# Performance work log

Measured on AMD Instinct MI355X. Metric: run time of the kernel, lower is better.

The kernel has to match this reference:

```python
import jax, jax.numpy as jnp
import numpy as np

LN_EPS = 1e-5


def setup_inputs() -> dict:
    key = jax.random.key(0)
    ks = jax.random.split(key, 7)
    B, L, D, H = 1, 4096, 512, 8  # batch must be 1; d_k=d_v=d_model (see source's double-bmm)
    q = jax.random.normal(ks[0], (B, L, D), jnp.float32)
    k = jax.random.normal(ks[1], (B, L, D), jnp.float32)
    v = jax.random.normal(ks[2], (B, L, D), jnp.float32)
    # causal mask: True = masked (filled with -inf), guarantees no fully-masked row
    attn_mask = jnp.triu(jnp.ones((L, L), dtype=bool), k=1)[None]  # (1, L, L)
    # xavier-normal-ish init for per-head projections (H, d_model, d_k)
    wscale = np.float32(np.sqrt(2.0 / (D + D)))
    w_qs = jax.random.normal(ks[3], (H, D, D), jnp.float32) * wscale
    w_ks = jax.random.normal(ks[4], (H, D, D), jnp.float32) * wscale
    w_vs = jax.random.normal(ks[5], (H, D, D), jnp.float32) * wscale
    pscale = np.float32(np.sqrt(2.0 / (H * D + D)))
    proj_w = jax.random.normal(ks[6], (D, H * D), jnp.float32) * pscale  # Linear(H*d_v, d_model)
    proj_b = jnp.zeros((D,), jnp.float32)
    ln_gamma = jnp.ones((D,), jnp.float32)
    ln_beta = jnp.zeros((D,), jnp.float32)
    return dict(q=q, k=k, v=v, attn_mask=attn_mask, w_qs=w_qs, w_ks=w_ks, w_vs=w_vs,
                proj_w=proj_w, proj_b=proj_b, ln_gamma=ln_gamma, ln_beta=ln_beta)


def reference(q, k, v, attn_mask, w_qs, w_ks, w_vs, proj_w, proj_b, ln_gamma, ln_beta):
    H, D, Dk = w_qs.shape          # d_k == d_model (required by source's duplicated bmm)
    B, Lq, _ = q.shape             # B == 1 (required by source's duplicated bmm)
    temper = jnp.sqrt(jnp.asarray(D, q.dtype))

    def proj_twice(x, w):
        # first projection: repeat over heads then bmm -> (H, B*L, Dk) -> view (H*B, L, Dk)
        xs = jnp.einsum('bld,hdk->hblk', x, w).reshape(H * B, -1, Dk)
        # duplicated second projection (faithful to the source code)
        return jnp.einsum('hlm,hmk->hlk', xs, w)  # (H, L, Dk)

    q_s = proj_twice(q, w_qs)
    k_s = proj_twice(k, w_ks)
    v_s = proj_twice(v, w_vs)

    # naive attention: full (H, Lq, Lk) score matrix materialized
    scores = jnp.einsum('hqd,hkd->hqk', q_s, k_s) / temper
    mask = jnp.broadcast_to(attn_mask, scores.shape)  # mask.repeat(n_head,1,1) with B=1
    scores = jnp.where(mask, -jnp.inf, scores)
    attn = jax.nn.softmax(scores, axis=-1)            # dropout = identity (eval mode)
    heads = jnp.einsum('hqk,hkd->hqd', attn, v_s)     # (H, Lq, Dv)

    # split along batch dim then cat along feature dim == (B, Lq, H*Dv)
    out = heads.transpose(1, 0, 2).reshape(B, Lq, H * Dk)
    out = out @ proj_w.T + proj_b                     # final Linear; dropout = identity

    x = out + q                                       # residual
    mu = jnp.mean(x, axis=-1, keepdims=True)
    var = jnp.var(x, axis=-1, keepdims=True)
    out = (x - mu) / jnp.sqrt(var + LN_EPS) * ln_gamma + ln_beta
    return out, attn
```

## Files before the change

kernel.cpp:

```cpp
#include <hip/hip_runtime.h>


typedef _Float16 f16;
typedef __attribute__((ext_vector_type(8))) _Float16 half8;
typedef __attribute__((ext_vector_type(4))) float float4v;

#define LSEQ 4096
#define DMODEL 512
#define NHEAD 8
#define BKK 64
#define LDSK (BKK + 8)

__device__ __forceinline__ half8 load8h(const f16* p) { return *(const half8*)p; }
__device__ __forceinline__ half8 load8h(const float* p) {
    float4 a = *(const float4*)p;
    float4 b = *(const float4*)(p + 4);
    half8 r;
    r[0] = (f16)a.x; r[1] = (f16)a.y; r[2] = (f16)a.z; r[3] = (f16)a.w;
    r[4] = (f16)b.x; r[5] = (f16)b.y; r[6] = (f16)b.z; r[7] = (f16)b.w;
    return r;
}

template<typename TA, typename TB, int BLAYOUT, int OUTMODE, bool KLIMIT>
__launch_bounds__(256)
__global__ void gemm64_kernel(const TA* __restrict__ A,
                              const TB* __restrict__ B,
                              void* __restrict__ Cv,
                              int M, int N, int K,
                              int ldA, int ldB, int ldC,
                              long sA, long sB, long sC,
                              float scale)
{
    const int bz = blockIdx.z;
    const int n0 = blockIdx.x * 64;
    const int m0 = blockIdx.y * 64;
    const int tid  = threadIdx.x;
    const int lane = tid & 63;
    const int wave = tid >> 6;
    const int wr = wave >> 1, wc = wave & 1;
    const int quad = lane >> 4, lr = lane & 15;

    if (OUTMODE == 2) {
        if (n0 >= m0 + 64) {
            float* Cb = (float*)Cv + (long)bz * sC;
            const float ninf = -__builtin_inff();
            float4 vv = make_float4(ninf, ninf, ninf, ninf);
            int r = tid >> 2, c = (tid & 3) * 16;
            #pragma unroll
            for (int j = 0; j < 4; j++)
                *(float4*)&Cb[(long)(m0 + r) * ldC + n0 + c + j * 4] = vv;
            return;
        }
    }

    __shared__ __align__(16) f16 Asm[64 * LDSK];
    __shared__ __align__(16) f16 Bsm[64 * LDSK];

    A += (long)bz * sA;
    B += (long)bz * sB;

    float4v acc[2][2];
    #pragma unroll
    for (int i = 0; i < 2; i++)
        #pragma unroll
        for (int j = 0; j < 2; j++) acc[i][j] = (float4v)0.0f;

    int kend = K;
    if (KLIMIT) kend = min(K, m0 + 64);

    const int rA = tid >> 3;
    const int cA = (tid & 7) * 8;

    for (int k0 = 0; k0 < kend; k0 += BKK) {
        {
            half8 v0 = load8h(&A[(long)(m0 + rA)      * ldA + k0 + cA]);
            half8 v1 = load8h(&A[(long)(m0 + rA + 32) * ldA + k0 + cA]);
            *(half8*)&Asm[ rA       * LDSK + cA] = v0;
            *(half8*)&Asm[(rA + 32) * LDSK + cA] = v1;
        }
        if (BLAYOUT == 0) {
            half8 v0 = load8h(&B[(long)(n0 + rA)      * ldB + k0 + cA]);
            half8 v1 = load8h(&B[(long)(n0 + rA + 32) * ldB + k0 + cA]);
            *(half8*)&Bsm[ rA       * LDSK + cA] = v0;
            *(half8*)&Bsm[(rA + 32) * LDSK + cA] = v1;
        } else {
            half8 v0 = load8h(&B[(long)(k0 + rA)      * ldB + n0 + cA]);
            half8 v1 = load8h(&B[(long)(k0 + rA + 32) * ldB + n0 + cA]);
            #pragma unroll
            for (int j = 0; j < 8; j++) {
                Bsm[(cA + j) * LDSK + rA     ] = v0[j];
                Bsm[(cA + j) * LDSK + rA + 32] = v1[j];
            }
        }
        __syncthreads();

        #pragma unroll
        for (int ks = 0; ks < 2; ks++) {
            half8 af[2], bfv[2];
            #pragma unroll
            for (int mt = 0; mt < 2; mt++)
                af[mt] = *(const half8*)&Asm[(wr * 32 + mt * 16 + lr) * LDSK + ks * 32 + quad * 8];
            #pragma unroll
            for (int nt = 0; nt < 2; nt++)
                bfv[nt] = *(const half8*)&Bsm[(wc * 32 + nt * 16 + lr) * LDSK + ks * 32 + quad * 8];
            #pragma unroll
            for (int mt = 0; mt < 2; mt++)
                #pragma unroll
                for (int nt = 0; nt < 2; nt++)
                    acc[mt][nt] = __builtin_amdgcn_mfma_f32_16x16x32_f16(
                        af[mt], bfv[nt], acc[mt][nt], 0, 0, 0);
        }
        __syncthreads();
    }

    #pragma unroll
    for (int mt = 0; mt < 2; mt++) {
        #pragma unroll
        for (int nt = 0; nt < 2; nt++) {
            #pragma unroll
            for (int r = 0; r < 4; r++) {
                int row = m0 + wr * 32 + mt * 16 + quad * 4 + r;
                int col = n0 + wc * 32 + nt * 16 + lr;
                float val = acc[mt][nt][r] * scale;
                if (OUTMODE == 0) {
                    f16* Cb = (f16*)Cv + (long)bz * sC;
                    Cb[(long)row * ldC + col] = (f16)val;
                } else if (OUTMODE == 1) {
                    float* Cb = (float*)Cv + (long)bz * sC;
                    Cb[(long)row * ldC + col] = val;
                } else {
                    float* Cb = (float*)Cv + (long)bz * sC;
                    if (col > row) val = -__builtin_inff();
                    Cb[(long)row * ldC + col] = val;
                }
            }
        }
    }
}

__launch_bounds__(256)
__global__ void softmax_kernel(float* __restrict__ attn)
{
    __shared__ float s[LSEQ];
    __shared__ float red[8];
    const long row = blockIdx.x;
    float* p = attn + row * (long)LSEQ;
    const int tid = threadIdx.x;

    float lmax = -__builtin_inff();
    #pragma unroll
    for (int i = 0; i < 4; i++) {
        float4 v = *(const float4*)&p[tid * 16 + i * 4];
        s[tid * 16 + i * 4 + 0] = v.x;
        s[tid * 16 + i * 4 + 1] = v.y;
        s[tid * 16 + i * 4 + 2] = v.z;
        s[tid * 16 + i * 4 + 3] = v.w;
        lmax = fmaxf(lmax, fmaxf(fmaxf(v.x, v.y), fmaxf(v.z, v.w)));
    }
    #pragma unroll
    for (int off = 32; off > 0; off >>= 1) lmax = fmaxf(lmax, __shfl_down(lmax, off));
    if ((tid & 63) == 0) red[tid >> 6] = lmax;
    __syncthreads();
    const float m = fmaxf(fmaxf(red[0], red[1]), fmaxf(red[2], red[3]));
    __syncthreads();

    float lsum = 0.0f;
    #pragma unroll
    for (int j = 0; j < 16; j++) {
        float e = __expf(s[tid * 16 + j] - m);
        s[tid * 16 + j] = e;
        lsum += e;
    }
    #pragma unroll
    for (int off = 32; off > 0; off >>= 1) lsum += __shfl_down(lsum, off);
    if ((tid & 63) == 0) red[tid >> 6] = lsum;
    __syncthreads();
    const float inv = 1.0f / (red[0] + red[1] + red[2] + red[3]);

    #pragma unroll
    for (int i = 0; i < 4; i++) {
        float4 o;
        o.x = s[tid * 16 + i * 4 + 0] * inv;
        o.y = s[tid * 16 + i * 4 + 1] * inv;
        o.z = s[tid * 16 + i * 4 + 2] * inv;
        o.w = s[tid * 16 + i * 4 + 3] * inv;
        *(float4*)&p[tid * 16 + i * 4] = o;
    }
}

__launch_bounds__(256)
__global__ void ln_kernel(float* lin_out,
                          const float* __restrict__ qin,
                          const float* __restrict__ bias,
                          const float* __restrict__ gamma,
                          const float* __restrict__ beta)
{
    __shared__ float red[8];
    const int l = blockIdx.x;
    const int tid = threadIdx.x;
    float* pl = lin_out + (long)l * DMODEL;
    const float* pq = qin + (long)l * DMODEL;

    float x0 = pl[tid]       + pq[tid]       + bias[tid];
    float x1 = pl[tid + 256] + pq[tid + 256] + bias[tid + 256];
    float sum = x0 + x1, sq = x0 * x0 + x1 * x1;
    #pragma unroll
    for (int off = 32; off > 0; off >>= 1) {
        sum += __shfl_down(sum, off);
        sq  += __shfl_down(sq,  off);
    }
    if ((tid & 63) == 0) { red[tid >> 6] = sum; red[4 + (tid >> 6)] = sq; }
    __syncthreads();
    const float S  = red[0] + red[1] + red[2] + red[3];
    const float Q2 = red[4] + red[5] + red[6] + red[7];
    const float mu = S * (1.0f / DMODEL);
    const float var = Q2 * (1.0f / DMODEL) - mu * mu;
    const float rstd = rsqrtf(var + 1e-5f);

    pl[tid]       = (x0 - mu) * rstd * gamma[tid]       + beta[tid];
    pl[tid + 256] = (x1 - mu) * rstd * gamma[tid + 256] + beta[tid + 256];
}

extern "C" void kernel_launch(void* const* d_in, const int* in_sizes, int n_in,
                              void* d_out, int out_size, void* d_ws, size_t ws_size,
                              hipStream_t stream)
{
    const float* q      = (const float*)d_in[0];
    const float* k      = (const float*)d_in[1];
    const float* v      = (const float*)d_in[2];
    const float* w_qs   = (const float*)d_in[4];
    const float* w_ks   = (const float*)d_in[5];
    const float* w_vs   = (const float*)d_in[6];
    const float* proj_w = (const float*)d_in[7];
    const float* proj_b = (const float*)d_in[8];
    const float* gamma  = (const float*)d_in[9];
    const float* beta   = (const float*)d_in[10];

    float* out  = (float*)d_out;
    float* attn = (float*)d_out + (long)LSEQ * DMODEL;

    const long PROJ = (long)NHEAD * LSEQ * DMODEL;
    char* ws = (char*)d_ws;
    f16* q_s   = (f16*)ws;  ws += PROJ * 2;
    f16* k_s   = (f16*)ws;  ws += PROJ * 2;
    f16* v_s   = (f16*)ws;  ws += PROJ * 2;
    f16* heads = (f16*)ws;

    f16* w2 = (f16*)d_out;

    const dim3 blk(256);
    const float inv_temper = 0.044194173824159216f;
    const long sW  = (long)DMODEL * DMODEL;
    const long sT  = (long)LSEQ * DMODEL;

    const dim3 gW(DMODEL / 64, DMODEL / 64, NHEAD);
    const dim3 gP(DMODEL / 64, LSEQ / 64, NHEAD);
    gemm64_kernel<float, float, 1, 0, false><<<gW, blk, 0, stream>>>(w_qs, w_qs, w2,  DMODEL, DMODEL, DMODEL, DMODEL, DMODEL, DMODEL, sW, sW, sW, 1.0f);
    gemm64_kernel<float, f16,   1, 0, false><<<gP, blk, 0, stream>>>(q,    w2,   q_s, LSEQ,   DMODEL, DMODEL, DMODEL, DMODEL, DMODEL, 0,  sW, sT, 1.0f);
    gemm64_kernel<float, float, 1, 0, false><<<gW, blk, 0, stream>>>(w_ks, w_ks, w2,  DMODEL, DMODEL, DMODEL, DMODEL, DMODEL, DMODEL, sW, sW, sW, 1.0f);
    gemm64_kernel<float, f16,   1, 0, false><<<gP, blk, 0, stream>>>(k,    w2,   k_s, LSEQ,   DMODEL, DMODEL, DMODEL, DMODEL, DMODEL, 0,  sW, sT, 1.0f);
    gemm64_kernel<float, float, 1, 0, false><<<gW, blk, 0, stream>>>(w_vs, w_vs, w2,  DMODEL, DMODEL, DMODEL, DMODEL, DMODEL, DMODEL, sW, sW, sW, 1.0f);
    gemm64_kernel<float, f16,   1, 0, false><<<gP, blk, 0, stream>>>(v,    w2,   v_s, LSEQ,   DMODEL, DMODEL, DMODEL, DMODEL, DMODEL, 0,  sW, sT, 1.0f);

    const dim3 gS(LSEQ / 64, LSEQ / 64, NHEAD);
    gemm64_kernel<f16, f16, 0, 2, false><<<gS, blk, 0, stream>>>(
        q_s, k_s, attn, LSEQ, LSEQ, DMODEL,
        DMODEL, DMODEL, LSEQ,
        sT, sT, (long)LSEQ * LSEQ, inv_temper);

    softmax_kernel<<<dim3(NHEAD * LSEQ), blk, 0, stream>>>(attn);

    gemm64_kernel<float, f16, 1, 0, true><<<dim3(DMODEL / 64, LSEQ / 64, NHEAD), blk, 0, stream>>>(
        attn, v_s, heads, LSEQ, DMODEL, LSEQ,
        LSEQ, DMODEL, NHEAD * DMODEL,
        (long)LSEQ * LSEQ, sT, (long)DMODEL, 1.0f);

    gemm64_kernel<f16, float, 0, 1, false><<<dim3(DMODEL / 64, LSEQ / 64, 1), blk, 0, stream>>>(
        heads, proj_w, out, LSEQ, DMODEL, NHEAD * DMODEL,
        NHEAD * DMODEL, NHEAD * DMODEL, DMODEL,
        0, 0, 0, 1.0f);

    ln_kernel<<<dim3(LSEQ), blk, 0, stream>>>(out, q, proj_b, gamma, beta);
}
```

Baseline: 1.775 ms.

## Fuse softmax with P·V product and store V projection transposed

Replaces the separate softmax and attn·V GEMM kernels with one kernel. Each block takes 32 query rows of one head, computes the row max and sum online over the causal range only, then writes normalized probabilities back and feeds them as fp16 through LDS into MFMA against a transposed V. The V projection now writes its output transposed so the fused kernel can read contiguous key-dimension slices. Fully masked score tiles are now written as zeros rather than -inf, which matches the final softmax output. The aim is to cut the repeated reads and writes of the 512MB score matrix and skip the masked upper triangle. The cost is that each block computes a full 512-wide output per row tile, and the transposed scattered fp16 stores in the V projection are uncoalesced.

```diff
diff --git a/kernel.cpp b/kernel.cpp
--- a/kernel.cpp
+++ b/kernel.cpp
@@ -43,8 +43,7 @@
     if (OUTMODE == 2) {
         if (n0 >= m0 + 64) {
             float* Cb = (float*)Cv + (long)bz * sC;
-            const float ninf = -__builtin_inff();
-            float4 vv = make_float4(ninf, ninf, ninf, ninf);
+            float4 vv = make_float4(0.0f, 0.0f, 0.0f, 0.0f);
             int r = tid >> 2, c = (tid & 3) * 16;
             #pragma unroll
             for (int j = 0; j < 4; j++)
@@ -128,6 +127,9 @@
                 } else if (OUTMODE == 1) {
                     float* Cb = (float*)Cv + (long)bz * sC;
                     Cb[(long)row * ldC + col] = val;
+                } else if (OUTMODE == 3) {
+                    f16* Cb = (f16*)Cv + (long)bz * sC;
+                    Cb[(long)col * ldC + row] = (f16)val;
                 } else {
                     float* Cb = (float*)Cv + (long)bz * sC;
                     if (col > row) val = -__builtin_inff();
@@ -139,53 +141,105 @@
 }
 
 __launch_bounds__(256)
-__global__ void softmax_kernel(float* __restrict__ attn)
+__global__ void softmax_pv_kernel(float* __restrict__ attn,
+                                  const f16* __restrict__ vT,
+                                  f16* __restrict__ heads)
 {
-    __shared__ float s[LSEQ];
-    __shared__ float red[8];
-    const long row = blockIdx.x;
-    float* p = attn + row * (long)LSEQ;
-    const int tid = threadIdx.x;
-
-    float lmax = -__builtin_inff();
-    #pragma unroll
-    for (int i = 0; i < 4; i++) {
-        float4 v = *(const float4*)&p[tid * 16 + i * 4];
-        s[tid * 16 + i * 4 + 0] = v.x;
-        s[tid * 16 + i * 4 + 1] = v.y;
-        s[tid * 16 + i * 4 + 2] = v.z;
-        s[tid * 16 + i * 4 + 3] = v.w;
-        lmax = fmaxf(lmax, fmaxf(fmaxf(v.x, v.y), fmaxf(v.z, v.w)));
-    }
-    #pragma unroll
-    for (int off = 32; off > 0; off >>= 1) lmax = fmaxf(lmax, __shfl_down(lmax, off));
-    if ((tid & 63) == 0) red[tid >> 6] = lmax;
+    int g = blockIdx.x;
+    int mb, h;
+    if (g < 512) { mb = g >> 2;                 h = g & 3; }
+    else         { g -= 512; mb = 127 - (g >> 2); h = 4 + (g & 3); }
+    const int m0 = mb * 32;
+    const int KE = (m0 & ~63) + 64;
+
+    const int tid  = threadIdx.x;
+    const int lane = tid & 63;
+    const int wc   = tid >> 6;
+    const int quad = lane >> 4, lr = lane & 15;
+
+    __shared__ __align__(16) f16 Psm[32 * LDSK];
+    __shared__ float mrow[32], isrow[32];
+
+    float* S = attn + (long)h * LSEQ * LSEQ;
+    const int r   = tid >> 3;
+    const int sub = tid & 7;
+    float* prow = S + (long)(m0 + r) * LSEQ;
+
+    float mt = -1e30f, st = 0.0f;
+    for (int k = sub * 8; k < KE; k += 64) {
+        float4 a = *(const float4*)&prow[k];
+        float4 b = *(const float4*)&prow[k + 4];
+        float mx = fmaxf(fmaxf(fmaxf(a.x, a.y), fmaxf(a.z, a.w)),
+                         fmaxf(fmaxf(b.x, b.y), fmaxf(b.z, b.w)));
+        if (mx > mt) { st *= __expf(mt - mx); mt = mx; }
+        st += __expf(a.x - mt) + __expf(a.y - mt) + __expf(a.z - mt) + __expf(a.w - mt)
+            + __expf(b.x - mt) + __expf(b.y - mt) + __expf(b.z - mt) + __expf(b.w - mt);
+    }
+    #pragma unroll
+    for (int off = 1; off < 8; off <<= 1) {
+        float mo = __shfl_xor(mt, off);
+        float so = __shfl_xor(st, off);
+        float mn = fmaxf(mt, mo);
+        st = st * __expf(mt - mn) + so * __expf(mo - mn);
+        mt = mn;
+    }
+    if (sub == 0) { mrow[r] = mt; isrow[r] = 1.0f / st; }
     __syncthreads();
-    const float m = fmaxf(fmaxf(red[0], red[1]), fmaxf(red[2], red[3]));
-    __syncthreads();
-
-    float lsum = 0.0f;
-    #pragma unroll
-    for (int j = 0; j < 16; j++) {
-        float e = __expf(s[tid * 16 + j] - m);
-        s[tid * 16 + j] = e;
-        lsum += e;
-    }
-    #pragma unroll
-    for (int off = 32; off > 0; off >>= 1) lsum += __shfl_down(lsum, off);
-    if ((tid & 63) == 0) red[tid >> 6] = lsum;
-    __syncthreads();
-    const float inv = 1.0f / (red[0] + red[1] + red[2] + red[3]);
-
-    #pragma unroll
-    for (int i = 0; i < 4; i++) {
-        float4 o;
-        o.x = s[tid * 16 + i * 4 + 0] * inv;
-        o.y = s[tid * 16 + i * 4 + 1] * inv;
-        o.z = s[tid * 16 + i * 4 + 2] * inv;
-        o.w = s[tid * 16 + i * 4 + 3] * inv;
-        *(float4*)&p[tid * 16 + i * 4] = o;
-    }
+    const float m_r = mrow[r], is_r = isrow[r];
+
+    float4v acc[2][8];
+    #pragma unroll
+    for (int i = 0; i < 2; i++)
+        #pragma unroll
+        for (int j = 0; j < 8; j++) acc[i][j] = (float4v)0.0f;
+
+    for (int kt = 0; kt < KE; kt += 64) {
+        float* pk = prow + kt + sub * 8;
+        float4 a = *(const float4*)pk;
+        float4 b = *(const float4*)(pk + 4);
+        a.x = __expf(a.x - m_r) * is_r;  a.y = __expf(a.y - m_r) * is_r;
+        a.z = __expf(a.z - m_r) * is_r;  a.w = __expf(a.w - m_r) * is_r;
+        b.x = __expf(b.x - m_r) * is_r;  b.y = __expf(b.y - m_r) * is_r;
+        b.z = __expf(b.z - m_r) * is_r;  b.w = __expf(b.w - m_r) * is_r;
+        *(float4*)pk = a;
+        *(float4*)(pk + 4) = b;
+        half8 hp;
+        hp[0] = (f16)a.x; hp[1] = (f16)a.y; hp[2] = (f16)a.z; hp[3] = (f16)a.w;
+        hp[4] = (f16)b.x; hp[5] = (f16)b.y; hp[6] = (f16)b.z; hp[7] = (f16)b.w;
+        *(half8*)&Psm[r * LDSK + sub * 8] = hp;
+        __syncthreads();
+
+        half8 af[2][2];
+        #pragma unroll
+        for (int m2 = 0; m2 < 2; m2++)
+            #pragma unroll
+            for (int ks = 0; ks < 2; ks++)
+                af[m2][ks] = *(const half8*)&Psm[(m2 * 16 + lr) * LDSK + ks * 32 + quad * 8];
+
+        const f16* vb = vT + ((long)h * DMODEL + wc * 128) * LSEQ + kt + quad * 8;
+        #pragma unroll
+        for (int nt = 0; nt < 8; nt++) {
+            const f16* vp = vb + (long)(nt * 16 + lr) * LSEQ;
+            half8 b0 = *(const half8*)vp;
+            half8 b1 = *(const half8*)(vp + 32);
+            acc[0][nt] = __builtin_amdgcn_mfma_f32_16x16x32_f16(af[0][0], b0, acc[0][nt], 0, 0, 0);
+            acc[0][nt] = __builtin_amdgcn_mfma_f32_16x16x32_f16(af[0][1], b1, acc[0][nt], 0, 0, 0);
+            acc[1][nt] = __builtin_amdgcn_mfma_f32_16x16x32_f16(af[1][0], b0, acc[1][nt], 0, 0, 0);
+            acc[1][nt] = __builtin_amdgcn_mfma_f32_16x16x32_f16(af[1][1], b1, acc[1][nt], 0, 0, 0);
+        }
+        __syncthreads();
+    }
+
+    #pragma unroll
+    for (int m2 = 0; m2 < 2; m2++)
+        #pragma unroll
+        for (int nt = 0; nt < 8; nt++)
+            #pragma unroll
+            for (int rr = 0; rr < 4; rr++) {
+                int row = m0 + m2 * 16 + quad * 4 + rr;
+                int col = wc * 128 + nt * 16 + lr;
+                heads[(long)row * (NHEAD * DMODEL) + h * DMODEL + col] = (f16)acc[m2][nt][rr];
+            }
 }
 
 __launch_bounds__(256)
@@ -243,7 +297,7 @@
     char* ws = (char*)d_ws;
     f16* q_s   = (f16*)ws;  ws += PROJ * 2;
     f16* k_s   = (f16*)ws;  ws += PROJ * 2;
-    f16* v_s   = (f16*)ws;  ws += PROJ * 2;
+    f16* v_sT  = (f16*)ws;  ws += PROJ * 2;
     f16* heads = (f16*)ws;
 
     f16* w2 = (f16*)d_out;
@@ -260,7 +314,7 @@
     gemm64_kernel<float, float, 1, 0, false><<<gW, blk, 0, stream>>>(w_ks, w_ks, w2,  DMODEL, DMODEL, DMODEL, DMODEL, DMODEL, DMODEL, sW, sW, sW, 1.0f);
     gemm64_kernel<float, f16,   1, 0, false><<<gP, blk, 0, stream>>>(k,    w2,   k_s, LSEQ,   DMODEL, DMODEL, DMODEL, DMODEL, DMODEL, 0,  sW, sT, 1.0f);
     gemm64_kernel<float, float, 1, 0, false><<<gW, blk, 0, stream>>>(w_vs, w_vs, w2,  DMODEL, DMODEL, DMODEL, DMODEL, DMODEL, DMODEL, sW, sW, sW, 1.0f);
-    gemm64_kernel<float, f16,   1, 0, false><<<gP, blk, 0, stream>>>(v,    w2,   v_s, LSEQ,   DMODEL, DMODEL, DMODEL, DMODEL, DMODEL, 0,  sW, sT, 1.0f);
+    gemm64_kernel<float, f16,   1, 3, false><<<gP, blk, 0, stream>>>(v,    w2,   v_sT, LSEQ,  DMODEL, DMODEL, DMODEL, DMODEL, LSEQ,   0,  sW, sT, 1.0f);
 
     const dim3 gS(LSEQ / 64, LSEQ / 64, NHEAD);
     gemm64_kernel<f16, f16, 0, 2, false><<<gS, blk, 0, stream>>>(
@@ -268,12 +322,7 @@
         DMODEL, DMODEL, LSEQ,
         sT, sT, (long)LSEQ * LSEQ, inv_temper);
 
-    softmax_kernel<<<dim3(NHEAD * LSEQ), blk, 0, stream>>>(attn);
-
-    gemm64_kernel<float, f16, 1, 0, true><<<dim3(DMODEL / 64, LSEQ / 64, NHEAD), blk, 0, stream>>>(
-        attn, v_s, heads, LSEQ, DMODEL, LSEQ,
-        LSEQ, DMODEL, NHEAD * DMODEL,
-        (long)LSEQ * LSEQ, sT, (long)DMODEL, 1.0f);
+    softmax_pv_kernel<<<dim3(128 * NHEAD), blk, 0, stream>>>(attn, v_sT, heads);
 
     gemm64_kernel<f16, float, 0, 1, false><<<dim3(DMODEL / 64, LSEQ / 64, 1), blk, 0, stream>>>(
         heads, proj_w, out, LSEQ, DMODEL, NHEAD * DMODEL,
```

Measured after the change: 1.552 ms. 12.6% less time.

## Fuse QK^T, softmax and PV into a two-pass flash-style attention kernel

Applied to the files above, without the earlier changes.

Replaces the separate score GEMM, row softmax kernel and attn×V GEMM with a single kernel per 32-row query block and head. The kernel computes the row max and sum in a first pass over causal key tiles, then recomputes scores, writes the normalized attention probabilities and accumulates P·V with MFMA in a second pass. The V projection now writes a transposed V, and the temperature scale is folded into the Q projection. The aim is to avoid reading back the full fp32 score matrix for softmax and again for PV, and to skip masked tiles beyond the diagonal except for zero-filling them. In exchange, QK^T is computed twice, and K and V are loaded directly from global memory without shared-memory staging.

```diff
diff --git a/kernel.cpp b/kernel.cpp
--- a/kernel.cpp
+++ b/kernel.cpp
@@ -10,6 +10,10 @@
 #define NHEAD 8
 #define BKK 64
 #define LDSK (BKK + 8)
+#define QLD (DMODEL + 8)
+#define PLD (128 + 8)
+#define MASKV -3.0e38f
+#define MINIT -1.0e30f
 
 __device__ __forceinline__ half8 load8h(const f16* p) { return *(const half8*)p; }
 __device__ __forceinline__ half8 load8h(const float* p) {
@@ -21,7 +25,7 @@
     return r;
 }
 
-template<typename TA, typename TB, int BLAYOUT, int OUTMODE, bool KLIMIT>
+template<typename TA, typename TB, int BLAYOUT, int OUTMODE>
 __launch_bounds__(256)
 __global__ void gemm64_kernel(const TA* __restrict__ A,
                               const TB* __restrict__ B,
@@ -40,19 +44,6 @@
     const int wr = wave >> 1, wc = wave & 1;
     const int quad = lane >> 4, lr = lane & 15;
 
-    if (OUTMODE == 2) {
-        if (n0 >= m0 + 64) {
-            float* Cb = (float*)Cv + (long)bz * sC;
-            const float ninf = -__builtin_inff();
-            float4 vv = make_float4(ninf, ninf, ninf, ninf);
-            int r = tid >> 2, c = (tid & 3) * 16;
-            #pragma unroll
-            for (int j = 0; j < 4; j++)
-                *(float4*)&Cb[(long)(m0 + r) * ldC + n0 + c + j * 4] = vv;
-            return;
-        }
-    }
-
     __shared__ __align__(16) f16 Asm[64 * LDSK];
     __shared__ __align__(16) f16 Bsm[64 * LDSK];
 
@@ -65,13 +56,10 @@
         #pragma unroll
         for (int j = 0; j < 2; j++) acc[i][j] = (float4v)0.0f;
 
-    int kend = K;
-    if (KLIMIT) kend = min(K, m0 + 64);
-
     const int rA = tid >> 3;
     const int cA = (tid & 7) * 8;
 
-    for (int k0 = 0; k0 < kend; k0 += BKK) {
+    for (int k0 = 0; k0 < K; k0 += BKK) {
         {
             half8 v0 = load8h(&A[(long)(m0 + rA)      * ldA + k0 + cA]);
             half8 v1 = load8h(&A[(long)(m0 + rA + 32) * ldA + k0 + cA]);
@@ -113,6 +101,25 @@
         __syncthreads();
     }
 
+    if (OUTMODE == 3) {
+        #pragma unroll
+        for (int mt = 0; mt < 2; mt++)
+            #pragma unroll
+            for (int nt = 0; nt < 2; nt++)
+                #pragma unroll
+                for (int r = 0; r < 4; r++) {
+                    int rl = wr * 32 + mt * 16 + quad * 4 + r;
+                    int cl = wc * 32 + nt * 16 + lr;
+                    Asm[cl * LDSK + rl] = (f16)(acc[mt][nt][r] * scale);
+                }
+        __syncthreads();
+        f16* Cb = (f16*)Cv + (long)bz * sC;
+        int cl = tid >> 2, rch = (tid & 3) * 16;
+        *(half8*)&Cb[(long)(n0 + cl) * ldC + m0 + rch]     = *(const half8*)&Asm[cl * LDSK + rch];
+        *(half8*)&Cb[(long)(n0 + cl) * ldC + m0 + rch + 8] = *(const half8*)&Asm[cl * LDSK + rch + 8];
+        return;
+    }
+
     #pragma unroll
     for (int mt = 0; mt < 2; mt++) {
         #pragma unroll
@@ -125,12 +132,8 @@
                 if (OUTMODE == 0) {
                     f16* Cb = (f16*)Cv + (long)bz * sC;
                     Cb[(long)row * ldC + col] = (f16)val;
-                } else if (OUTMODE == 1) {
-                    float* Cb = (float*)Cv + (long)bz * sC;
-                    Cb[(long)row * ldC + col] = val;
                 } else {
                     float* Cb = (float*)Cv + (long)bz * sC;
-                    if (col > row) val = -__builtin_inff();
                     Cb[(long)row * ldC + col] = val;
                 }
             }
@@ -139,53 +142,215 @@
 }
 
 __launch_bounds__(256)
-__global__ void softmax_kernel(float* __restrict__ attn)
+__global__ void flash_kernel(const f16* __restrict__ q_s,
+                             const f16* __restrict__ k_s,
+                             const f16* __restrict__ vT,
+                             float* __restrict__ attn,
+                             f16* __restrict__ heads)
 {
-    __shared__ float s[LSEQ];
-    __shared__ float red[8];
-    const long row = blockIdx.x;
-    float* p = attn + row * (long)LSEQ;
-    const int tid = threadIdx.x;
-
-    float lmax = -__builtin_inff();
-    #pragma unroll
-    for (int i = 0; i < 4; i++) {
-        float4 v = *(const float4*)&p[tid * 16 + i * 4];
-        s[tid * 16 + i * 4 + 0] = v.x;
-        s[tid * 16 + i * 4 + 1] = v.y;
-        s[tid * 16 + i * 4 + 2] = v.z;
-        s[tid * 16 + i * 4 + 3] = v.w;
-        lmax = fmaxf(lmax, fmaxf(fmaxf(v.x, v.y), fmaxf(v.z, v.w)));
-    }
-    #pragma unroll
-    for (int off = 32; off > 0; off >>= 1) lmax = fmaxf(lmax, __shfl_down(lmax, off));
-    if ((tid & 63) == 0) red[tid >> 6] = lmax;
+    const int g = blockIdx.x;
+    const int h = g & 7;
+    const int j = g >> 3;
+    const int mb = (j & 1) ? (127 - (j >> 1)) : (j >> 1);
+    const int m0 = mb * 32;
+    const int KE2 = (m0 & ~127) + 128;
+
+    const int tid  = threadIdx.x;
+    const int w    = tid >> 6;
+    const int lane = tid & 63;
+    const int quad = lane >> 4, lr = lane & 15;
+
+    __shared__ __align__(16) f16 Qsm[32 * QLD];
+    __shared__ __align__(16) f16 Psm[2][32 * PLD];
+    __shared__ float warrM[4][32], warrL[4][32];
+    __shared__ float mrow[32], isrow[32];
+
+    const long sT  = (long)LSEQ * DMODEL;
+    float* A = attn + (long)h * LSEQ * LSEQ;
+
+    {
+        const int zr = tid >> 3, zc = (tid & 7) * 16;
+        const float4 z = make_float4(0.0f, 0.0f, 0.0f, 0.0f);
+        for (int kt = KE2; kt < LSEQ; kt += 128) {
+            float* p = A + (long)(m0 + zr) * LSEQ + kt + zc;
+            *(float4*)p = z; *(float4*)(p + 4) = z;
+            *(float4*)(p + 8) = z; *(float4*)(p + 12) = z;
+        }
+    }
+
+    {
+        const f16* qp = q_s + (long)h * sT + (long)m0 * DMODEL;
+        const int rq = tid >> 3, cq = (tid & 7) * 8;
+        #pragma unroll
+        for (int jj = 0; jj < 8; jj++)
+            *(half8*)&Qsm[rq * QLD + cq + jj * 64] =
+                *(const half8*)&qp[(long)rq * DMODEL + cq + jj * 64];
+    }
     __syncthreads();
-    const float m = fmaxf(fmaxf(red[0], red[1]), fmaxf(red[2], red[3]));
+
+    const f16* kbase = k_s + (long)h * sT + (long)(32 * w + lr) * DMODEL;
+
+    float m8[8], l8[8];
+    #pragma unroll
+    for (int i = 0; i < 8; i++) { m8[i] = MINIT; l8[i] = 0.0f; }
+
+    for (int kt = 0; kt < KE2; kt += 128) {
+        float4v s[2][2];
+        #pragma unroll
+        for (int mf = 0; mf < 2; mf++)
+            #pragma unroll
+            for (int nf = 0; nf < 2; nf++) s[mf][nf] = (float4v)0.0f;
+
+        const f16* kp0 = kbase + (long)kt * DMODEL;
+        const f16* kp1 = kp0 + 16 * DMODEL;
+        #pragma unroll
+        for (int ks = 0; ks < 16; ks++) {
+            half8 a0 = *(const half8*)&Qsm[lr        * QLD + ks * 32 + quad * 8];
+            half8 a1 = *(const half8*)&Qsm[(lr + 16) * QLD + ks * 32 + quad * 8];
+            half8 b0 = *(const half8*)&kp0[ks * 32 + quad * 8];
+            half8 b1 = *(const half8*)&kp1[ks * 32 + quad * 8];
+            s[0][0] = __builtin_amdgcn_mfma_f32_16x16x32_f16(a0, b0, s[0][0], 0, 0, 0);
+            s[0][1] = __builtin_amdgcn_mfma_f32_16x16x32_f16(a0, b1, s[0][1], 0, 0, 0);
+            s[1][0] = __builtin_amdgcn_mfma_f32_16x16x32_f16(a1, b0, s[1][0], 0, 0, 0);
+            s[1][1] = __builtin_amdgcn_mfma_f32_16x16x32_f16(a1, b1, s[1][1], 0, 0, 0);
+        }
+        const bool domask = (kt + 128 == KE2);
+        #pragma unroll
+        for (int mf = 0; mf < 2; mf++)
+            #pragma unroll
+            for (int nf = 0; nf < 2; nf++)
+                #pragma unroll
+                for (int rr = 0; rr < 4; rr++) {
+                    float v = s[mf][nf][rr];
+                    if (domask &&
+                        (kt + 32 * w + 16 * nf + lr > m0 + 16 * mf + quad * 4 + rr))
+                        v = MASKV;
+                    const int i = mf * 4 + rr;
+                    if (v <= m8[i]) {
+                        l8[i] += __expf(v - m8[i]);
+                    } else {
+                        l8[i] = l8[i] * __expf(m8[i] - v) + 1.0f;
+                        m8[i] = v;
+                    }
+                }
+    }
+
+    #pragma unroll
+    for (int off = 1; off < 16; off <<= 1) {
+        #pragma unroll
+        for (int i = 0; i < 8; i++) {
+            float mo = __shfl_xor(m8[i], off);
+            float lo = __shfl_xor(l8[i], off);
+            float nm = fmaxf(m8[i], mo);
+            l8[i] = l8[i] * __expf(m8[i] - nm) + lo * __expf(mo - nm);
+            m8[i] = nm;
+        }
+    }
+    if (lr == 0) {
+        #pragma unroll
+        for (int i = 0; i < 8; i++) {
+            const int rl = 16 * (i >> 2) + quad * 4 + (i & 3);
+            warrM[w][rl] = m8[i]; warrL[w][rl] = l8[i];
+        }
+    }
     __syncthreads();
-
-    float lsum = 0.0f;
-    #pragma unroll
-    for (int j = 0; j < 16; j++) {
-        float e = __expf(s[tid * 16 + j] - m);
-        s[tid * 16 + j] = e;
-        lsum += e;
-    }
-    #pragma unroll
-    for (int off = 32; off > 0; off >>= 1) lsum += __shfl_down(lsum, off);
-    if ((tid & 63) == 0) red[tid >> 6] = lsum;
+    if (tid < 32) {
+        float m = MINIT, l = 0.0f;
+        #pragma unroll
+        for (int ww = 0; ww < 4; ww++) {
+            float mo = warrM[ww][tid], lo = warrL[ww][tid];
+            float nm = fmaxf(m, mo);
+            l = l * __expf(m - nm) + lo * __expf(mo - nm);
+            m = nm;
+        }
+        mrow[tid] = m; isrow[tid] = 1.0f / l;
+    }
     __syncthreads();
-    const float inv = 1.0f / (red[0] + red[1] + red[2] + red[3]);
-
-    #pragma unroll
-    for (int i = 0; i < 4; i++) {
-        float4 o;
-        o.x = s[tid * 16 + i * 4 + 0] * inv;
-        o.y = s[tid * 16 + i * 4 + 1] * inv;
-        o.z = s[tid * 16 + i * 4 + 2] * inv;
-        o.w = s[tid * 16 + i * 4 + 3] * inv;
-        *(float4*)&p[tid * 16 + i * 4] = o;
-    }
+
+    float mf8[8], if8[8];
+    #pragma unroll
+    for (int i = 0; i < 8; i++) {
+        const int rl = 16 * (i >> 2) + quad * 4 + (i & 3);
+        mf8[i] = mrow[rl]; if8[i] = isrow[rl];
+    }
+
+    float4v acc[2][8];
+    #pragma unroll
+    for (int mf = 0; mf < 2; mf++)
+        #pragma unroll
+        for (int nt = 0; nt < 8; nt++) acc[mf][nt] = (float4v)0.0f;
+
+    int buf = 0;
+    for (int kt = 0; kt < KE2; kt += 128) {
+        float4v s[2][2];
+        #pragma unroll
+        for (int mf = 0; mf < 2; mf++)
+            #pragma unroll
+            for (int nf = 0; nf < 2; nf++) s[mf][nf] = (float4v)0.0f;
+
+        const f16* kp0 = kbase + (long)kt * DMODEL;
+        const f16* kp1 = kp0 + 16 * DMODEL;
+        #pragma unroll
+        for (int ks = 0; ks < 16; ks++) {
+            half8 a0 = *(const half8*)&Qsm[lr        * QLD + ks * 32 + quad * 8];
+            half8 a1 = *(const half8*)&Qsm[(lr + 16) * QLD + ks * 32 + quad * 8];
+            half8 b0 = *(const half8*)&kp0[ks * 32 + quad * 8];
+            half8 b1 = *(const half8*)&kp1[ks * 32 + quad * 8];
+            s[0][0] = __builtin_amdgcn_mfma_f32_16x16x32_f16(a0, b0, s[0][0], 0, 0, 0);
+            s[0][1] = __builtin_amdgcn_mfma_f32_16x16x32_f16(a0, b1, s[0][1], 0, 0, 0);
+            s[1][0] = __builtin_amdgcn_mfma_f32_16x16x32_f16(a1, b0, s[1][0], 0, 0, 0);
+            s[1][1] = __builtin_amdgcn_mfma_f32_16x16x32_f16(a1, b1, s[1][1], 0, 0, 0);
+        }
+        const bool domask = (kt + 128 == KE2);
+        #pragma unroll
+        for (int mf = 0; mf < 2; mf++)
+            #pragma unroll
+            for (int nf = 0; nf < 2; nf++)
+                #pragma unroll
+                for (int rr = 0; rr < 4; rr++) {
+                    float v = s[mf][nf][rr];
+                    if (domask &&
+                        (kt + 32 * w + 16 * nf + lr > m0 + 16 * mf + quad * 4 + rr))
+                        v = MASKV;
+                    const int i = mf * 4 + rr;
+                    const float p = __expf(v - mf8[i]) * if8[i];
+                    const int rl = 16 * mf + quad * 4 + rr;
+                    A[(long)(m0 + rl) * LSEQ + kt + 32 * w + 16 * nf + lr] = p;
+                    Psm[buf][rl * PLD + 32 * w + 16 * nf + lr] = (f16)p;
+                }
+        __syncthreads();
+
+        half8 af[2][4];
+        #pragma unroll
+        for (int mf = 0; mf < 2; mf++)
+            #pragma unroll
+            for (int ksv = 0; ksv < 4; ksv++)
+                af[mf][ksv] = *(const half8*)&Psm[buf][(16 * mf + lr) * PLD + ksv * 32 + quad * 8];
+
+        const f16* vbase = vT + ((long)h * DMODEL + 128 * w) * LSEQ + kt;
+        #pragma unroll
+        for (int nt = 0; nt < 8; nt++) {
+            const f16* vp = vbase + (long)(nt * 16 + lr) * LSEQ;
+            #pragma unroll
+            for (int ksv = 0; ksv < 4; ksv++) {
+                half8 bv = *(const half8*)&vp[ksv * 32 + quad * 8];
+                acc[0][nt] = __builtin_amdgcn_mfma_f32_16x16x32_f16(af[0][ksv], bv, acc[0][nt], 0, 0, 0);
+                acc[1][nt] = __builtin_amdgcn_mfma_f32_16x16x32_f16(af[1][ksv], bv, acc[1][nt], 0, 0, 0);
+            }
+        }
+        buf ^= 1;
+    }
+
+    #pragma unroll
+    for (int mf = 0; mf < 2; mf++)
+        #pragma unroll
+        for (int nt = 0; nt < 8; nt++)
+            #pragma unroll
+            for (int rr = 0; rr < 4; rr++) {
+                const int row = m0 + 16 * mf + quad * 4 + rr;
+                const int col = 128 * w + nt * 16 + lr;
+                heads[(long)row * (NHEAD * DMODEL) + h * DMODEL + col] = (f16)acc[mf][nt][rr];
+            }
 }
 
 __launch_bounds__(256)
@@ -243,7 +408,7 @@
     char* ws = (char*)d_ws;
     f16* q_s   = (f16*)ws;  ws += PROJ * 2;
     f16* k_s   = (f16*)ws;  ws += PROJ * 2;
-    f16* v_s   = (f16*)ws;  ws += PROJ * 2;
+    f16* v_sT  = (f16*)ws;  ws += PROJ * 2;
     f16* heads = (f16*)ws;
 
     f16* w2 = (f16*)d_out;
@@ -255,27 +420,16 @@
 
     const dim3 gW(DMODEL / 64, DMODEL / 64, NHEAD);
     const dim3 gP(DMODEL / 64, LSEQ / 64, NHEAD);
-    gemm64_kernel<float, float, 1, 0, false><<<gW, blk, 0, stream>>>(w_qs, w_qs, w2,  DMODEL, DMODEL, DMODEL, DMODEL, DMODEL, DMODEL, sW, sW, sW, 1.0f);
-    gemm64_kernel<float, f16,   1, 0, false><<<gP, blk, 0, stream>>>(q,    w2,   q_s, LSEQ,   DMODEL, DMODEL, DMODEL, DMODEL, DMODEL, 0,  sW, sT, 1.0f);
-    gemm64_kernel<float, float, 1, 0, false><<<gW, blk, 0, stream>>>(w_ks, w_ks, w2,  DMODEL, DMODEL, DMODEL, DMODEL, DMODEL, DMODEL, sW, sW, sW, 1.0f);
-    gemm64_kernel<float, f16,   1, 0, false><<<gP, blk, 0, stream>>>(k,    w2,   k_s, LSEQ,   DMODEL, DMODEL, DMODEL, DMODEL, DMODEL, 0,  sW, sT, 1.0f);
-    gemm64_kernel<float, float, 1, 0, false><<<gW, blk, 0, stream>>>(w_vs, w_vs, w2,  DMODEL, DMODEL, DMODEL, DMODEL, DMODEL, DMODEL, sW, sW, sW, 1.0f);
-    gemm64_kernel<float, f16,   1, 0, false><<<gP, blk, 0, stream>>>(v,    w2,   v_s, LSEQ,   DMODEL, DMODEL, DMODEL, DMODEL, DMODEL, 0,  sW, sT, 1.0f);
-
-    const dim3 gS(LSEQ / 64, LSEQ / 64, NHEAD);
-    gemm64_kernel<f16, f16, 0, 2, false><<<gS, blk, 0, stream>>>(
-        q_s, k_s, attn, LSEQ, LSEQ, DMODEL,
-        DMODEL, DMODEL, LSEQ,
-        sT, sT, (long)LSEQ * LSEQ, inv_temper);
-
-    softmax_kernel<<<dim3(NHEAD * LSEQ), blk, 0, stream>>>(attn);
-
-    gemm64_kernel<float, f16, 1, 0, true><<<dim3(DMODEL / 64, LSEQ / 64, NHEAD), blk, 0, stream>>>(
-        attn, v_s, heads, LSEQ, DMODEL, LSEQ,
-        LSEQ, DMODEL, NHEAD * DMODEL,
-        (long)LSEQ * LSEQ, sT, (long)DMODEL, 1.0f);
-
-    gemm64_kernel<f16, float, 0, 1, false><<<dim3(DMODEL / 64, LSEQ / 64, 1), blk, 0, stream>>>(
+    gemm64_kernel<float, float, 1, 0><<<gW, blk, 0, stream>>>(w_qs, w_qs, w2,  DMODEL, DMODEL, DMODEL, DMODEL, DMODEL, DMODEL, sW, sW, sW, 1.0f);
+    gemm64_kernel<float, f16,   1, 0><<<gP, blk, 0, stream>>>(q,    w2,   q_s, LSEQ,   DMODEL, DMODEL, DMODEL, DMODEL, DMODEL, 0,  sW, sT, inv_temper);
+    gemm64_kernel<float, float, 1, 0><<<gW, blk, 0, stream>>>(w_ks, w_ks, w2,  DMODEL, DMODEL, DMODEL, DMODEL, DMODEL, DMODEL, sW, sW, sW, 1.0f);
+    gemm64_kernel<float, f16,   1, 0><<<gP, blk, 0, stream>>>(k,    w2,   k_s, LSEQ,   DMODEL, DMODEL, DMODEL, DMODEL, DMODEL, 0,  sW, sT, 1.0f);
+    gemm64_kernel<float, float, 1, 0><<<gW, blk, 0, stream>>>(w_vs, w_vs, w2,  DMODEL, DMODEL, DMODEL, DMODEL, DMODEL, DMODEL, sW, sW, sW, 1.0f);
+    gemm64_kernel<float, f16,   1, 3><<<gP, blk, 0, stream>>>(v,    w2,   v_sT, LSEQ,  DMODEL, DMODEL, DMODEL, DMODEL, LSEQ,   0,  sW, sT, 1.0f);
+
+    flash_kernel<<<dim3(128 * NHEAD), blk, 0, stream>>>(q_s, k_s, v_sT, attn, heads);
+
+    gemm64_kernel<f16, float, 0, 1><<<dim3(DMODEL / 64, LSEQ / 64, 1), blk, 0, stream>>>(
         heads, proj_w, out, LSEQ, DMODEL, NHEAD * DMODEL,
         NHEAD * DMODEL, NHEAD * DMODEL, DMODEL,
         0, 0, 0, 1.0f);
```

After: 2.685 ms. 51.2% more time.

## Fuse softmax normalization into PV kernel with per-row stats pass

Applied to the files above, without the earlier changes.

Replaces the full-row softmax kernel with a stats kernel that computes online max and inverse-sum only over the causal prefix, followed by a fused PV kernel. The PV kernel normalizes scores, writes the attention probabilities back in place and feeds them to MFMA against a transposed V. It also folds the temperature scale into the Q projection and writes zeros directly for masked tiles. This removes the separate read/write pass over the upper-triangular half of the 512MB attention matrix, at the cost of reading V from global memory without LDS reuse and a new transposed-output epilogue.

```diff
diff --git a/kernel.cpp b/kernel.cpp
--- a/kernel.cpp
+++ b/kernel.cpp
@@ -3,6 +3,7 @@
 
 typedef _Float16 f16;
 typedef __attribute__((ext_vector_type(8))) _Float16 half8;
+typedef __attribute__((ext_vector_type(4))) _Float16 half4;
 typedef __attribute__((ext_vector_type(4))) float float4v;
 
 #define LSEQ 4096
@@ -10,6 +11,8 @@
 #define NHEAD 8
 #define BKK 64
 #define LDSK (BKK + 8)
+#define PLD 80
+#define MINIT -1.0e30f
 
 __device__ __forceinline__ half8 load8h(const f16* p) { return *(const half8*)p; }
 __device__ __forceinline__ half8 load8h(const float* p) {
@@ -21,7 +24,7 @@
     return r;
 }
 
-template<typename TA, typename TB, int BLAYOUT, int OUTMODE, bool KLIMIT>
+template<typename TA, typename TB, int BLAYOUT, int OUTMODE>
 __launch_bounds__(256)
 __global__ void gemm64_kernel(const TA* __restrict__ A,
                               const TB* __restrict__ B,
@@ -43,8 +46,7 @@
     if (OUTMODE == 2) {
         if (n0 >= m0 + 64) {
             float* Cb = (float*)Cv + (long)bz * sC;
-            const float ninf = -__builtin_inff();
-            float4 vv = make_float4(ninf, ninf, ninf, ninf);
+            float4 vv = make_float4(0.0f, 0.0f, 0.0f, 0.0f);
             int r = tid >> 2, c = (tid & 3) * 16;
             #pragma unroll
             for (int j = 0; j < 4; j++)
@@ -65,13 +67,10 @@
         #pragma unroll
         for (int j = 0; j < 2; j++) acc[i][j] = (float4v)0.0f;
 
-    int kend = K;
-    if (KLIMIT) kend = min(K, m0 + 64);
-
     const int rA = tid >> 3;
     const int cA = (tid & 7) * 8;
 
-    for (int k0 = 0; k0 < kend; k0 += BKK) {
+    for (int k0 = 0; k0 < K; k0 += BKK) {
         {
             half8 v0 = load8h(&A[(long)(m0 + rA)      * ldA + k0 + cA]);
             half8 v1 = load8h(&A[(long)(m0 + rA + 32) * ldA + k0 + cA]);
@@ -113,6 +112,25 @@
         __syncthreads();
     }
 
+    if (OUTMODE == 3) {
+        #pragma unroll
+        for (int mt = 0; mt < 2; mt++)
+            #pragma unroll
+            for (int nt = 0; nt < 2; nt++)
+                #pragma unroll
+                for (int r = 0; r < 4; r++) {
+                    int rl = wr * 32 + mt * 16 + quad * 4 + r;
+                    int cl = wc * 32 + nt * 16 + lr;
+                    Asm[cl * LDSK + rl] = (f16)(acc[mt][nt][r] * scale);
+                }
+        __syncthreads();
+        f16* Cb = (f16*)Cv + (long)bz * sC;
+        int cl = tid >> 2, rch = (tid & 3) * 16;
+        *(half8*)&Cb[(long)(n0 + cl) * ldC + m0 + rch]     = *(const half8*)&Asm[cl * LDSK + rch];
+        *(half8*)&Cb[(long)(n0 + cl) * ldC + m0 + rch + 8] = *(const half8*)&Asm[cl * LDSK + rch + 8];
+        return;
+    }
+
     #pragma unroll
     for (int mt = 0; mt < 2; mt++) {
         #pragma unroll
@@ -125,12 +143,12 @@
                 if (OUTMODE == 0) {
                     f16* Cb = (f16*)Cv + (long)bz * sC;
                     Cb[(long)row * ldC + col] = (f16)val;
-                } else if (OUTMODE == 1) {
+                } else if (OUTMODE == 2) {
                     float* Cb = (float*)Cv + (long)bz * sC;
+                    if (col > row) val = -__builtin_inff();
                     Cb[(long)row * ldC + col] = val;
                 } else {
                     float* Cb = (float*)Cv + (long)bz * sC;
-                    if (col > row) val = -__builtin_inff();
                     Cb[(long)row * ldC + col] = val;
                 }
             }
@@ -139,53 +157,110 @@
 }
 
 __launch_bounds__(256)
-__global__ void softmax_kernel(float* __restrict__ attn)
-{
-    __shared__ float s[LSEQ];
-    __shared__ float red[8];
-    const long row = blockIdx.x;
-    float* p = attn + row * (long)LSEQ;
-    const int tid = threadIdx.x;
-
-    float lmax = -__builtin_inff();
-    #pragma unroll
-    for (int i = 0; i < 4; i++) {
-        float4 v = *(const float4*)&p[tid * 16 + i * 4];
-        s[tid * 16 + i * 4 + 0] = v.x;
-        s[tid * 16 + i * 4 + 1] = v.y;
-        s[tid * 16 + i * 4 + 2] = v.z;
-        s[tid * 16 + i * 4 + 3] = v.w;
-        lmax = fmaxf(lmax, fmaxf(fmaxf(v.x, v.y), fmaxf(v.z, v.w)));
-    }
-    #pragma unroll
-    for (int off = 32; off > 0; off >>= 1) lmax = fmaxf(lmax, __shfl_down(lmax, off));
-    if ((tid & 63) == 0) red[tid >> 6] = lmax;
+__global__ void stats_kernel(const float* __restrict__ attn,
+                             float2* __restrict__ ml)
+{
+    const int rl   = (blockIdx.x << 2) + (threadIdx.x >> 6);
+    const int lane = threadIdx.x & 63;
+    const int h = rl >> 12;
+    const int r = rl & (LSEQ - 1);
+    const float* p = attn + (long)h * LSEQ * LSEQ + (long)r * LSEQ;
+    const int KE = (r & ~63) + 64;
+
+    float m = MINIT, l = 0.0f;
+    for (int k = lane * 8; k < KE; k += 512) {
+        float4 a = *(const float4*)&p[k];
+        float4 b = *(const float4*)&p[k + 4];
+        float mx = fmaxf(fmaxf(fmaxf(a.x, a.y), fmaxf(a.z, a.w)),
+                         fmaxf(fmaxf(b.x, b.y), fmaxf(b.z, b.w)));
+        if (mx > m) { l *= __expf(m - mx); m = mx; }
+        l += __expf(a.x - m) + __expf(a.y - m) + __expf(a.z - m) + __expf(a.w - m)
+           + __expf(b.x - m) + __expf(b.y - m) + __expf(b.z - m) + __expf(b.w - m);
+    }
+    #pragma unroll
+    for (int off = 1; off < 64; off <<= 1) {
+        float mo = __shfl_xor(m, off);
+        float lo = __shfl_xor(l, off);
+        float nm = fmaxf(m, mo);
+        l = l * __expf(m - nm) + lo * __expf(mo - nm);
+        m = nm;
+    }
+    if (lane == 0) ml[rl] = make_float2(m, 1.0f / l);
+}
+
+__launch_bounds__(256)
+__global__ void pv_kernel(float* __restrict__ attn,
+                          const f16* __restrict__ vT,
+                          const float2* __restrict__ ml,
+                          f16* __restrict__ heads)
+{
+    const int x = blockIdx.x;
+    const int h = blockIdx.y;
+    const int mb = (x & 1) ? (255 - (x >> 1)) : (x >> 1);
+    const int m0 = mb * 16;
+    const int KE = (m0 & ~63) + 64;
+
+    const int tid  = threadIdx.x;
+    const int w    = tid >> 6;
+    const int lane = tid & 63;
+    const int quad = lane >> 4, lr = lane & 15;
+
+    __shared__ __align__(16) f16 Psm[2][16 * PLD];
+    __shared__ float mrow[16], irow[16];
+
+    if (tid < 16) {
+        float2 s = ml[h * LSEQ + m0 + tid];
+        mrow[tid] = s.x; irow[tid] = s.y;
+    }
     __syncthreads();
-    const float m = fmaxf(fmaxf(red[0], red[1]), fmaxf(red[2], red[3]));
-    __syncthreads();
-
-    float lsum = 0.0f;
-    #pragma unroll
-    for (int j = 0; j < 16; j++) {
-        float e = __expf(s[tid * 16 + j] - m);
-        s[tid * 16 + j] = e;
-        lsum += e;
-    }
-    #pragma unroll
-    for (int off = 32; off > 0; off >>= 1) lsum += __shfl_down(lsum, off);
-    if ((tid & 63) == 0) red[tid >> 6] = lsum;
-    __syncthreads();
-    const float inv = 1.0f / (red[0] + red[1] + red[2] + red[3]);
-
-    #pragma unroll
-    for (int i = 0; i < 4; i++) {
-        float4 o;
-        o.x = s[tid * 16 + i * 4 + 0] * inv;
-        o.y = s[tid * 16 + i * 4 + 1] * inv;
-        o.z = s[tid * 16 + i * 4 + 2] * inv;
-        o.w = s[tid * 16 + i * 4 + 3] * inv;
-        *(float4*)&p[tid * 16 + i * 4] = o;
-    }
+
+    float* A = attn + (long)h * LSEQ * LSEQ;
+    const int pr = tid >> 4;
+    const int pc = (tid & 15) * 4;
+    const float m_r = mrow[pr], i_r = irow[pr];
+
+    float4v acc[8];
+    #pragma unroll
+    for (int i = 0; i < 8; i++) acc[i] = (float4v)0.0f;
+
+    const f16* vbase = vT + ((long)h * DMODEL + 128 * w) * LSEQ;
+
+    int buf = 0;
+    for (int kt = 0; kt < KE; kt += 64) {
+        float* pp = A + (long)(m0 + pr) * LSEQ + kt + pc;
+        float4 a = *(const float4*)pp;
+        a.x = __expf(a.x - m_r) * i_r;
+        a.y = __expf(a.y - m_r) * i_r;
+        a.z = __expf(a.z - m_r) * i_r;
+        a.w = __expf(a.w - m_r) * i_r;
+        *(float4*)pp = a;
+        half4 hp;
+        hp[0] = (f16)a.x; hp[1] = (f16)a.y; hp[2] = (f16)a.z; hp[3] = (f16)a.w;
+        *(half4*)&Psm[buf][pr * PLD + pc] = hp;
+        __syncthreads();
+
+        half8 af0 = *(const half8*)&Psm[buf][lr * PLD + quad * 8];
+        half8 af1 = *(const half8*)&Psm[buf][lr * PLD + 32 + quad * 8];
+        const f16* vp = vbase + kt + quad * 8;
+        #pragma unroll
+        for (int nt = 0; nt < 8; nt++) {
+            const f16* vrow = vp + (long)(nt * 16 + lr) * LSEQ;
+            half8 b0 = *(const half8*)vrow;
+            half8 b1 = *(const half8*)(vrow + 32);
+            acc[nt] = __builtin_amdgcn_mfma_f32_16x16x32_f16(af0, b0, acc[nt], 0, 0, 0);
+            acc[nt] = __builtin_amdgcn_mfma_f32_16x16x32_f16(af1, b1, acc[nt], 0, 0, 0);
+        }
+        buf ^= 1;
+    }
+
+    #pragma unroll
+    for (int nt = 0; nt < 8; nt++)
+        #pragma unroll
+        for (int rr = 0; rr < 4; rr++) {
+            const int row = m0 + quad * 4 + rr;
+            const int col = 128 * w + nt * 16 + lr;
+            heads[(long)row * (NHEAD * DMODEL) + h * DMODEL + col] = (f16)acc[nt][rr];
+        }
 }
 
 __launch_bounds__(256)
@@ -243,10 +318,11 @@
     char* ws = (char*)d_ws;
     f16* q_s   = (f16*)ws;  ws += PROJ * 2;
     f16* k_s   = (f16*)ws;  ws += PROJ * 2;
-    f16* v_s   = (f16*)ws;  ws += PROJ * 2;
+    f16* v_sT  = (f16*)ws;  ws += PROJ * 2;
     f16* heads = (f16*)ws;
 
-    f16* w2 = (f16*)d_out;
+    f16* w2    = (f16*)d_out;
+    float2* ml = (float2*)((char*)d_out + (4 << 20));
 
     const dim3 blk(256);
     const float inv_temper = 0.044194173824159216f;
@@ -255,27 +331,24 @@
 
     const dim3 gW(DMODEL / 64, DMODEL / 64, NHEAD);
     const dim3 gP(DMODEL / 64, LSEQ / 64, NHEAD);
-    gemm64_kernel<float, float, 1, 0, false><<<gW, blk, 0, stream>>>(w_qs, w_qs, w2,  DMODEL, DMODEL, DMODEL, DMODEL, DMODEL, DMODEL, sW, sW, sW, 1.0f);
-    gemm64_kernel<float, f16,   1, 0, false><<<gP, blk, 0, stream>>>(q,    w2,   q_s, LSEQ,   DMODEL, DMODEL, DMODEL, DMODEL, DMODEL, 0,  sW, sT, 1.0f);
-    gemm64_kernel<float, float, 1, 0, false><<<gW, blk, 0, stream>>>(w_ks, w_ks, w2,  DMODEL, DMODEL, DMODEL, DMODEL, DMODEL, DMODEL, sW, sW, sW, 1.0f);
-    gemm64_kernel<float, f16,   1, 0, false><<<gP, blk, 0, stream>>>(k,    w2,   k_s, LSEQ,   DMODEL, DMODEL, DMODEL, DMODEL, DMODEL, 0,  sW, sT, 1.0f);
-    gemm64_kernel<float, float, 1, 0, false><<<gW, blk, 0, stream>>>(w_vs, w_vs, w2,  DMODEL, DMODEL, DMODEL, DMODEL, DMODEL, DMODEL, sW, sW, sW, 1.0f);
-    gemm64_kernel<float, f16,   1, 0, false><<<gP, blk, 0, stream>>>(v,    w2,   v_s, LSEQ,   DMODEL, DMODEL, DMODEL, DMODEL, DMODEL, 0,  sW, sT, 1.0f);
+    gemm64_kernel<float, float, 1, 0><<<gW, blk, 0, stream>>>(w_qs, w_qs, w2,  DMODEL, DMODEL, DMODEL, DMODEL, DMODEL, DMODEL, sW, sW, sW, 1.0f);
+    gemm64_kernel<float, f16,   1, 0><<<gP, blk, 0, stream>>>(q,    w2,   q_s, LSEQ,   DMODEL, DMODEL, DMODEL, DMODEL, DMODEL, 0,  sW, sT, inv_temper);
+    gemm64_kernel<float, float, 1, 0><<<gW, blk, 0, stream>>>(w_ks, w_ks, w2,  DMODEL, DMODEL, DMODEL, DMODEL, DMODEL, DMODEL, sW, sW, sW, 1.0f);
+    gemm64_kernel<float, f16,   1, 0><<<gP, blk, 0, stream>>>(k,    w2,   k_s, LSEQ,   DMODEL, DMODEL, DMODEL, DMODEL, DMODEL, 0,  sW, sT, 1.0f);
+    gemm64_kernel<float, float, 1, 0><<<gW, blk, 0, stream>>>(w_vs, w_vs, w2,  DMODEL, DMODEL, DMODEL, DMODEL, DMODEL, DMODEL, sW, sW, sW, 1.0f);
+    gemm64_kernel<float, f16,   1, 3><<<gP, blk, 0, stream>>>(v,    w2,   v_sT, LSEQ,  DMODEL, DMODEL, DMODEL, DMODEL, LSEQ,   0,  sW, sT, 1.0f);
 
     const dim3 gS(LSEQ / 64, LSEQ / 64, NHEAD);
-    gemm64_kernel<f16, f16, 0, 2, false><<<gS, blk, 0, stream>>>(
+    gemm64_kernel<f16, f16, 0, 2><<<gS, blk, 0, stream>>>(
         q_s, k_s, attn, LSEQ, LSEQ, DMODEL,
         DMODEL, DMODEL, LSEQ,
-        sT, sT, (long)LSEQ * LSEQ, inv_temper);
-
-    softmax_kernel<<<dim3(NHEAD * LSEQ), blk, 0, stream>>>(attn);
-
-    gemm64_kernel<float, f16, 1, 0, true><<<dim3(DMODEL / 64, LSEQ / 64, NHEAD), blk, 0, stream>>>(
-        attn, v_s, heads, LSEQ, DMODEL, LSEQ,
-        LSEQ, DMODEL, NHEAD * DMODEL,
-        (long)LSEQ * LSEQ, sT, (long)DMODEL, 1.0f);
-
-    gemm64_kernel<f16, float, 0, 1, false><<<dim3(DMODEL / 64, LSEQ / 64, 1), blk, 0, stream>>>(
+        sT, sT, (long)LSEQ * LSEQ, 1.0f);
+
+    stats_kernel<<<dim3(NHEAD * LSEQ / 4), blk, 0, stream>>>(attn, ml);
+
+    pv_kernel<<<dim3(LSEQ / 16, NHEAD), blk, 0, stream>>>(attn, v_sT, ml, heads);
+
+    gemm64_kernel<f16, float, 0, 1><<<dim3(DMODEL / 64, LSEQ / 64, 1), blk, 0, stream>>>(
         heads, proj_w, out, LSEQ, DMODEL, NHEAD * DMODEL,
         NHEAD * DMODEL, NHEAD * DMODEL, DMODEL,
         0, 0, 0, 1.0f);
```

New measurement: 2.062 ms. +16.1%, slower.
